# Kernel optimization log

Hardware: AMD Instinct MI355X
Metric: run time of the kernel (lower is better)

Reference implementation:

```python
import jax, jax.numpy as jnp
import numpy as np

N = 8192      # atoms
E = 4096      # edges (become transformer tokens)
E2 = 65536    # edges of second graph y
VOCAB = 119
DE = 200      # node_features == embedding_dim
D = 256
H = 8
L = 2
DFF = 2048


def _bn(x, g, b, eps=1e-6):
    m = x.mean(0)
    v = x.var(0)
    return (x - m) * jax.lax.rsqrt(v + eps) * g + b


def _ln(x, g, b, eps=1e-5):
    m = x.mean(-1, keepdims=True)
    v = ((x - m) ** 2).mean(-1, keepdims=True)
    return (x - m) * jax.lax.rsqrt(v + eps) * g + b


def _gcn(x, ei, W, b):
    # PyG GCNConv: add self loops, symmetric deg^-1/2 normalization
    n = x.shape[0]
    loop = jnp.arange(n)
    src = jnp.concatenate([ei[0], loop])
    dst = jnp.concatenate([ei[1], loop])
    deg = jax.ops.segment_sum(jnp.ones(src.shape[0], x.dtype), dst, num_segments=n)
    dinv = jnp.where(deg > 0, jax.lax.rsqrt(jnp.maximum(deg, 1e-12)), 0.0)
    msg = (x @ W)[src] * (dinv[src] * dinv[dst])[:, None]
    return jax.ops.segment_sum(msg, dst, num_segments=n) + b


def _mha(x, wi, bi, wo, bo):
    S, d = x.shape
    dh = d // H
    q, k, v = jnp.split(x @ wi + bi, 3, axis=1)
    q = q.reshape(S, H, dh)
    k = k.reshape(S, H, dh)
    v = v.reshape(S, H, dh)
    sc = jnp.einsum('qhd,khd->hqk', q, k) * (1.0 / np.sqrt(dh))
    a = jax.nn.softmax(sc, axis=-1)
    o = jnp.einsum('hqk,khd->qhd', a, v).reshape(S, d)
    return o @ wo + bo


def setup_inputs() -> dict:
    key = jax.random.key(0)
    ks = iter(jax.random.split(key, 64))
    nrm = lambda shape, s=0.05: jax.random.normal(next(ks), shape, jnp.float32) * s
    d = {}
    d['x'] = jax.random.randint(next(ks), (N,), 0, VOCAB)
    d['edge_index'] = jax.random.randint(next(ks), (2, E), 1, N + 1)  # 1-based, code subtracts 1
    d['pos'] = jax.random.normal(next(ks), (N, 3), jnp.float32)
    d['y'] = jax.random.randint(next(ks), (2, E2), 0, E)
    d['emb'] = nrm((VOCAB, DE), 1.0)
    d['fc1_w'] = nrm((1, DE))
    d['fc1_b'] = jnp.zeros((DE,), jnp.float32)
    d['bn4_g'] = jnp.ones((DE,), jnp.float32)
    d['bn4_b'] = jnp.zeros((DE,), jnp.float32)
    d['conv1_w'] = nrm((DE, D))
    d['conv1_b'] = jnp.zeros((D,), jnp.float32)
    d['conv2_w'] = nrm((D, D))
    d['conv2_b'] = jnp.zeros((D,), jnp.float32)
    for i in (1, 2, 3):
        d['bn%d_g' % i] = jnp.ones((D,), jnp.float32)
        d['bn%d_b' % i] = jnp.zeros((D,), jnp.float32)
    d['in_proj_w'] = nrm((L, D, 3 * D))
    d['in_proj_b'] = jnp.zeros((L, 3 * D), jnp.float32)
    d['out_proj_w'] = nrm((L, D, D))
    d['out_proj_b'] = jnp.zeros((L, D), jnp.float32)
    d['ln1_g'] = jnp.ones((L, D), jnp.float32)
    d['ln1_b'] = jnp.zeros((L, D), jnp.float32)
    d['ln2_g'] = jnp.ones((L, D), jnp.float32)
    d['ln2_b'] = jnp.zeros((L, D), jnp.float32)
    d['ff1_w'] = nrm((L, D, DFF))
    d['ff1_b'] = jnp.zeros((L, DFF), jnp.float32)
    d['ff2_w'] = nrm((L, DFF, D))
    d['ff2_b'] = jnp.zeros((L, D), jnp.float32)
    d['fc3_w'] = nrm((D, 1))
    d['fc3_b'] = jnp.zeros((1,), jnp.float32)
    d['fc4_w'] = nrm((D, 9))
    d['fc4_b'] = jnp.zeros((9,), jnp.float32)
    return d


def reference(x, edge_index, pos, y, emb, fc1_w, fc1_b, bn4_g, bn4_b,
              conv1_w, conv1_b, conv2_w, conv2_b,
              bn1_g, bn1_b, bn2_g, bn2_b, bn3_g, bn3_b,
              in_proj_w, in_proj_b, out_proj_w, out_proj_b,
              ln1_g, ln1_b, ln2_g, ln2_b, ff1_w, ff1_b, ff2_w, ff2_b,
              fc3_w, fc3_b, fc4_w, fc4_b):
    h = emb[x]                                   # [N, DE]
    ei = edge_index - 1
    row, col = ei[0], ei[1]
    ef = jnp.linalg.norm(pos[col] - pos[row], axis=1, keepdims=True)  # [E,1]
    ef = _bn(ef @ fc1_w + fc1_b, bn4_g, bn4_b)   # [E, DE]
    h = h[row] + h[col] + ef                     # [E, DE] edges -> tokens
    h = jax.nn.leaky_relu(_gcn(h, y, conv1_w, conv1_b))
    h = _bn(h, bn1_g, bn1_b)
    h = jax.nn.leaky_relu(h + _gcn(h, y, conv2_w, conv2_b))
    h = _bn(h, bn2_g, bn2_b)
    # post-norm TransformerEncoder (unbatched seq of length E), dropout=0
    for i in range(L):
        h = _ln(h + _mha(h, in_proj_w[i], in_proj_b[i], out_proj_w[i], out_proj_b[i]),
                ln1_g[i], ln1_b[i])
        ff = jax.nn.relu(h @ ff1_w[i] + ff1_b[i]) @ ff2_w[i] + ff2_b[i]
        h = _ln(h + ff, ln2_g[i], ln2_b[i])
    h = jax.nn.leaky_relu(h)
    h = _bn(h, bn3_g, bn3_b)
    sym_out = h @ fc3_w + fc3_b
    asym_out = h @ fc4_w + fc4_b
    return (sym_out, asym_out)
```

## Files before the change

### kernel.cpp

```cpp
#include <hip/hip_runtime.h>
#include <math.h>

#define ETOK 4096
#define NE2  65536
#define DEF  200
#define DM   256
#define NH   8
#define DH   32
#define DFFN 2048
#define NKS  4

#define QSCALE_LOG2E 0.25503474f

typedef __attribute__((ext_vector_type(8))) short bfrag8;
typedef __attribute__((ext_vector_type(4))) float f32x4;
typedef __attribute__((ext_vector_type(4))) short short4v;
typedef __attribute__((ext_vector_type(4))) unsigned int u32x4;

__device__ __forceinline__ unsigned short f2bf(float f) {
  union { float f; unsigned u; } v; v.f = f;
  unsigned u = v.u + 0x7fffu + ((v.u >> 16) & 1u);
  return (unsigned short)(u >> 16);
}
__device__ __forceinline__ float bf2f(unsigned short u) {
  union { unsigned u; float f; } v;
  v.u = ((unsigned)u) << 16;
  return v.f;
}
__device__ __forceinline__ unsigned cvt_pk_bf16(float lo, float hi) {
  unsigned r;
  asm("v_cvt_pk_bf16_f32 %0, %1, %2" : "=v"(r) : "v"(lo), "v"(hi));
  return r;
}

__device__ __forceinline__ float wave_sum(float v) {
#pragma unroll
  for (int off = 32; off > 0; off >>= 1) v += __shfl_xor(v, off);
  return v;
}
__device__ __forceinline__ float block_sum(float v, float* red) {
  v = wave_sum(v);
  int lane = threadIdx.x & 63, w = threadIdx.x >> 6;
  if (lane == 0) red[w] = v;
  __syncthreads();
  float t = red[0] + red[1] + red[2] + red[3];
  __syncthreads();
  return t;
}

__global__ void edge_deg_kernel(const int* __restrict__ ei, const float* __restrict__ pos,
                                float* __restrict__ ef0, float* __restrict__ stats,
                                const int* __restrict__ y, int* __restrict__ deg) {
  __shared__ float red[4];
  int e2 = blockIdx.x * 256 + threadIdx.x;
  atomicAdd(&deg[y[NE2 + e2]], 1);
  if (blockIdx.x < 16) {
    int e = blockIdx.x * 256 + threadIdx.x;
    int r = ei[e] - 1;
    int c = ei[ETOK + e] - 1;
    float dx = pos[c * 3 + 0] - pos[r * 3 + 0];
    float dy = pos[c * 3 + 1] - pos[r * 3 + 1];
    float dz = pos[c * 3 + 2] - pos[r * 3 + 2];
    float d = sqrtf(dx * dx + dy * dy + dz * dz);
    ef0[e] = d;
    float s = block_sum(d, red);
    float s2 = block_sum(d * d, red);
    if (threadIdx.x == 0) {
      atomicAdd(stats + 0, s);
      atomicAdd(stats + 1, s2);
    }
  }
}

__global__ void token_build_kernel(const int* __restrict__ x, const int* __restrict__ ei,
                                   const float* __restrict__ emb, const float* __restrict__ fc1_w,
                                   const float* __restrict__ bn4_g, const float* __restrict__ bn4_b,
                                   const float* __restrict__ ef0, const float* __restrict__ stats,
                                   unsigned short* __restrict__ tokbf) {
  int e = blockIdx.x;
  int j = threadIdx.x;
  float m = stats[0] * (1.0f / 4096.0f);
  float v = stats[1] * (1.0f / 4096.0f) - m * m;
  int xr = x[ei[e] - 1];
  int xc = x[ei[ETOK + e] - 1];
  float dd = ef0[e] - m;
  float val = 0.f;
  if (j < DEF) {
    float w = fc1_w[j];
    float s = w * rsqrtf(v * w * w + 1e-6f) * bn4_g[j];
    val = emb[(size_t)xr * DEF + j] + emb[(size_t)xc * DEF + j] + dd * s + bn4_b[j];
  }
  tokbf[(size_t)e * 256 + j] = f2bf(val);
}

__global__ void scan_kernel(const int* __restrict__ deg, int* __restrict__ off,
                            int* __restrict__ cursor, float* __restrict__ dinv) {
  __shared__ int part[256];
  int t = threadIdx.x;
  int v[16];
  int s = 0;
#pragma unroll
  for (int i = 0; i < 16; ++i) {
    v[i] = deg[t * 16 + i];
    s += v[i];
  }
  part[t] = s;
  __syncthreads();
  if (t == 0) {
    int a = 0;
#pragma unroll 1
    for (int i = 0; i < 256; ++i) {
      int tmp = part[i];
      part[i] = a;
      a += tmp;
    }
    off[4096] = a;
  }
  __syncthreads();
  int a = part[t];
#pragma unroll
  for (int i = 0; i < 16; ++i) {
    off[t * 16 + i] = a;
    cursor[t * 16 + i] = a;
    dinv[t * 16 + i] = rsqrtf((float)(v[i] + 1));
    a += v[i];
  }
}
__global__ void fill_kernel(const int* __restrict__ y, int* __restrict__ cursor,
                            int* __restrict__ srcl) {
  int e = blockIdx.x * 256 + threadIdx.x;
  int s = y[e];
  int d = y[NE2 + e];
  int slot = atomicAdd(&cursor[d], 1);
  srcl[slot] = s;
}

template <int RES, int ACT>
__global__ __launch_bounds__(256) void gather_kernel(const float* __restrict__ xw,
                                                     const int* __restrict__ off,
                                                     const int* __restrict__ srcl,
                                                     const float* __restrict__ dinv,
                                                     const float* __restrict__ bias,
                                                     const float* __restrict__ resid,
                                                     float* __restrict__ out) {
  __shared__ int slds[256];
  __shared__ float dlds[256];
  const int d = blockIdx.x;
  const int c = threadIdx.x;
  const int b0 = off[d], b1 = off[d + 1];
  const float dd = dinv[d];
  float acc = 0.f;
  for (int base = b0; base < b1; base += 256) {
    int n = min(256, b1 - base);
    __syncthreads();
    if (c < n) {
      int s = srcl[base + c];
      slds[c] = s;
      dlds[c] = dinv[s];
    }
    __syncthreads();
    for (int j = 0; j < n; ++j) {
      int s = slds[j];
      acc = fmaf(xw[(size_t)s * DM + c], dlds[j], acc);
    }
  }
  size_t idx = (size_t)d * DM + c;
  float v = bias[c] + xw[idx] * dd * dd + acc * dd;
  if (RES) v += resid[idx];
  if (ACT) v = v > 0.f ? v : 0.01f * v;
  out[idx] = v;
}

struct WEntry {
  const float* src;
  unsigned short* dst;
  int K, N, KP, tilesN, ntiles;
};
struct WPack {
  WEntry e[10];
};
__global__ __launch_bounds__(256) void wtrans_all_kernel(WPack p) {
  __shared__ float tl[32][33];
  int t = blockIdx.x;
  int i = 0;
  while (t >= p.e[i].ntiles) {
    t -= p.e[i].ntiles;
    ++i;
  }
  const WEntry w = p.e[i];
  int nb = (t % w.tilesN) * 32;
  int kb = (t / w.tilesN) * 32;
  int tx = threadIdx.x & 31, ty = threadIdx.x >> 5;
#pragma unroll
  for (int r = ty; r < 32; r += 8) {
    int k = kb + r, n = nb + tx;
    tl[r][tx] = (k < w.K && n < w.N) ? w.src[(size_t)k * w.N + n] : 0.f;
  }
  __syncthreads();
#pragma unroll
  for (int r = ty; r < 32; r += 8) {
    int n = nb + r, k = kb + tx;
    if (n < w.N) w.dst[(size_t)n * w.KP + k] = f2bf(tl[tx][r]);
  }
}

template <int BM, int BN, int OUTBF, int ACT, int QS, int VSPLIT>
__global__ __launch_bounds__(256) void mfma_gemm(const unsigned short* __restrict__ A,
                                                 const unsigned short* __restrict__ Bt,
                                                 const float* __restrict__ bias,
                                                 void* __restrict__ Cout, void* __restrict__ Cout2,
                                                 int M, int N, int K) {
  constexpr int BK = 64;
  constexpr int TM = BM / 32, TN = BN / 32;
  constexpr int ACH = BM / 32, BCH = BN / 32;
  __shared__ unsigned short Alds[BM * BK];
  __shared__ unsigned short Blds[BN * BK];
  const int tid = threadIdx.x;
  const int lane = tid & 63, wid = tid >> 6;
  const int g = lane >> 4, q = lane & 15;
  const int wr = wid >> 1, wc = wid & 1;
  const int m0 = blockIdx.y * BM, n0 = blockIdx.x * BN;

  f32x4 acc[TM][TN];
#pragma unroll
  for (int i = 0; i < TM; ++i)
#pragma unroll
    for (int j = 0; j < TN; ++j) acc[i][j] = (f32x4){0.f, 0.f, 0.f, 0.f};

  for (int k0 = 0; k0 < K; k0 += BK) {
    __syncthreads();
#pragma unroll
    for (int c = 0; c < ACH; ++c) {
      int chunk = wid * ACH + c;
      int row = chunk * 8 + (lane >> 3);
      int cb = ((lane & 7) * 16) ^ ((row & 7) << 4);
      const char* gp = (const char*)A + ((size_t)(m0 + row) * K + k0) * 2 + cb;
      __builtin_amdgcn_global_load_lds(
          (const __attribute__((address_space(1))) unsigned int*)gp,
          (__attribute__((address_space(3))) unsigned int*)(Alds + chunk * 512), 16, 0, 0);
    }
#pragma unroll
    for (int c = 0; c < BCH; ++c) {
      int chunk = wid * BCH + c;
      int row = chunk * 8 + (lane >> 3);
      int cb = ((lane & 7) * 16) ^ ((row & 7) << 4);
      const char* gp = (const char*)Bt + ((size_t)(n0 + row) * K + k0) * 2 + cb;
      __builtin_amdgcn_global_load_lds(
          (const __attribute__((address_space(1))) unsigned int*)gp,
          (__attribute__((address_space(3))) unsigned int*)(Blds + chunk * 512), 16, 0, 0);
    }
    __syncthreads();
#pragma unroll
    for (int ks = 0; ks < 2; ++ks) {
      bfrag8 af[TM], bfr[TN];
#pragma unroll
      for (int mi = 0; mi < TM; ++mi) {
        int row = wr * (BM / 2) + mi * 16 + q;
        int cb = (ks * 64 + g * 16) ^ ((row & 7) << 4);
        af[mi] = *(const bfrag8*)((const char*)Alds + row * 128 + cb);
      }
#pragma unroll
      for (int ni = 0; ni < TN; ++ni) {
        int row = wc * (BN / 2) + ni * 16 + q;
        int cb = (ks * 64 + g * 16) ^ ((row & 7) << 4);
        bfr[ni] = *(const bfrag8*)((const char*)Blds + row * 128 + cb);
      }
#pragma unroll
      for (int mi = 0; mi < TM; ++mi)
#pragma unroll
        for (int ni = 0; ni < TN; ++ni)
          acc[mi][ni] = __builtin_amdgcn_mfma_f32_16x16x32_bf16(af[mi], bfr[ni], acc[mi][ni], 0, 0, 0);
    }
  }
#pragma unroll
  for (int mi = 0; mi < TM; ++mi) {
    int row = m0 + wr * (BM / 2) + mi * 16 + g * 4;
#pragma unroll
    for (int ni = 0; ni < TN; ++ni) {
      int col = n0 + wc * (BN / 2) + ni * 16 + q;
      float bv = bias ? bias[col] : 0.f;
      if (VSPLIT && col >= 512) {
        short4v pkv;
#pragma unroll
        for (int r = 0; r < 4; ++r) pkv[r] = (short)f2bf(acc[mi][ni][r] + bv);
        *(short4v*)((unsigned short*)Cout2 + (size_t)(col - 512) * M + row) = pkv;
      } else {
#pragma unroll
        for (int r = 0; r < 4; ++r) {
          float v = acc[mi][ni][r] + bv;
          if (QS && col < DM) v *= QSCALE_LOG2E;
          if (ACT == 1) v = fmaxf(v, 0.f);
          if (OUTBF)
            ((unsigned short*)Cout)[(size_t)(row + r) * (VSPLIT ? 512 : N) + col] = f2bf(v);
          else
            ((float*)Cout)[(size_t)(row + r) * N + col] = v;
        }
      }
    }
  }
}

template <int LEAKY>
__global__ __launch_bounds__(256) void col_accum_kernel(const float* __restrict__ x,
                                                        float* __restrict__ colm,
                                                        float* __restrict__ colv) {
  int c = threadIdx.x;
  int r0 = blockIdx.x * 16;
  float s = 0.f, s2 = 0.f;
#pragma unroll
  for (int i = 0; i < 16; ++i) {
    float v = x[(size_t)(r0 + i) * DM + c];
    if (LEAKY) v = v > 0.f ? v : 0.01f * v;
    s += v;
    s2 += v * v;
  }
  atomicAdd(&colm[c], s);
  atomicAdd(&colv[c], s2);
}
template <int LEAKY>
__global__ void bn_apply_kernel(const float* __restrict__ x, const float* __restrict__ colm,
                                const float* __restrict__ colv, const float* __restrict__ g,
                                const float* __restrict__ b, float* __restrict__ outf,
                                unsigned short* __restrict__ outb, int C) {
  size_t i = (size_t)blockIdx.x * 256 + threadIdx.x;
  int c = (int)(i % C);
  float mean = colm[c] * (1.0f / 4096.0f);
  float var = colv[c] * (1.0f / 4096.0f) - mean * mean;
  float v0 = x[i];
  if (LEAKY) v0 = v0 > 0.f ? v0 : 0.01f * v0;
  float v = (v0 - mean) * rsqrtf(var + 1e-6f) * g[c] + b[c];
  outf[i] = v;
  if (outb) outb[i] = f2bf(v);
}

__global__ __launch_bounds__(256, 4) void attn_mfma_kernel(const unsigned short* __restrict__ qk,
                                                           const unsigned short* __restrict__ vt,
                                                           unsigned short* __restrict__ Opart,
                                                           float* __restrict__ Lpart) {
  const int h = blockIdx.y;
  const int qblk = blockIdx.x * 128;
  const int chunk = blockIdx.z;
  const int tid = threadIdx.x;
  const int wid = tid >> 6, lane = tid & 63;
  const int g = lane >> 4, q = lane & 15;

  __shared__ unsigned short Klds[2][64][40];
  __shared__ unsigned int Vtw[2][32][36];
  __shared__ unsigned short Plds[4][32][72];

  bfrag8 qfrag0, qfrag1;
  {
    const unsigned short* qp = qk + (size_t)(qblk + wid * 32 + q) * 512 + h * DH + g * 8;
    qfrag0 = *(const bfrag8*)qp;
    qfrag1 = *(const bfrag8*)(qp + 16 * 512);
  }
  const f32x4 zero = {0.f, 0.f, 0.f, 0.f};

  const int skey = tid >> 2;
  const int sdb = (tid & 3) * 8;
  const int sd = tid >> 3;
  const int sk4 = (tid & 7) * 4;

  const int kbeg = chunk * (ETOK / NKS);
  const int NT = (ETOK / NKS) / 64;

  const unsigned short* kptr = qk + (size_t)(kbeg + skey) * 512 + DM + h * DH + sdb;
  const unsigned short* vptr = vt + (size_t)(h * DH + sd) * ETOK + kbeg + sk4 * 2;

  bfrag8 kreg = *(const bfrag8*)kptr;
  kptr += (size_t)64 * 512;
  u32x4 vreg = *(const u32x4*)vptr;
  vptr += 64;

  float lsum0 = 0.f, lsum1 = 0.f;
  f32x4 o00 = zero, o01 = zero, o10 = zero, o11 = zero;

  for (int t = 0; t < NT; ++t) {
    const int buf = t & 1;
    *(bfrag8*)&Klds[buf][skey][sdb] = kreg;
    *(u32x4*)&Vtw[buf][sd][sk4] = vreg;
    __syncthreads();
    if (t + 1 < NT) {
      kreg = *(const bfrag8*)kptr;
      kptr += (size_t)64 * 512;
      vreg = *(const u32x4*)vptr;
      vptr += 64;
    }

    f32x4 st0[4], st1[4];
    __builtin_amdgcn_s_setprio(1);
#pragma unroll
    for (int tt = 0; tt < 4; ++tt) {
      bfrag8 kf = *(const bfrag8*)&Klds[buf][tt * 16 + q][g * 8];
      st0[tt] = __builtin_amdgcn_mfma_f32_16x16x32_bf16(kf, qfrag0, zero, 0, 0, 0);
      st1[tt] = __builtin_amdgcn_mfma_f32_16x16x32_bf16(kf, qfrag1, zero, 0, 0, 0);
    }
    __builtin_amdgcn_s_setprio(0);

    {
      float ps = 0.f;
#pragma unroll
      for (int tt = 0; tt < 4; ++tt) {
        float p0 = __builtin_exp2f(st0[tt][0]);
        float p1 = __builtin_exp2f(st0[tt][1]);
        float p2 = __builtin_exp2f(st0[tt][2]);
        float p3 = __builtin_exp2f(st0[tt][3]);
        ps += (p0 + p1) + (p2 + p3);
        uint2 w2;
        w2.x = cvt_pk_bf16(p0, p1);
        w2.y = cvt_pk_bf16(p2, p3);
        *(uint2*)&Plds[wid][q][tt * 16 + g * 4] = w2;
      }
      lsum0 += ps;
    }
    {
      float ps = 0.f;
#pragma unroll
      for (int tt = 0; tt < 4; ++tt) {
        float p0 = __builtin_exp2f(st1[tt][0]);
        float p1 = __builtin_exp2f(st1[tt][1]);
        float p2 = __builtin_exp2f(st1[tt][2]);
        float p3 = __builtin_exp2f(st1[tt][3]);
        ps += (p0 + p1) + (p2 + p3);
        uint2 w2;
        w2.x = cvt_pk_bf16(p0, p1);
        w2.y = cvt_pk_bf16(p2, p3);
        *(uint2*)&Plds[wid][16 + q][tt * 16 + g * 4] = w2;
      }
      lsum1 += ps;
    }

    __builtin_amdgcn_s_setprio(1);
#pragma unroll
    for (int kg = 0; kg < 2; ++kg) {
      bfrag8 vb0 = *(const bfrag8*)&Vtw[buf][q][kg * 16 + g * 4];
      bfrag8 vb1 = *(const bfrag8*)&Vtw[buf][16 + q][kg * 16 + g * 4];
      bfrag8 pa0 = *(const bfrag8*)&Plds[wid][q][kg * 32 + g * 8];
      bfrag8 pa1 = *(const bfrag8*)&Plds[wid][16 + q][kg * 32 + g * 8];
      o00 = __builtin_amdgcn_mfma_f32_16x16x32_bf16(pa0, vb0, o00, 0, 0, 0);
      o01 = __builtin_amdgcn_mfma_f32_16x16x32_bf16(pa0, vb1, o01, 0, 0, 0);
      o10 = __builtin_amdgcn_mfma_f32_16x16x32_bf16(pa1, vb0, o10, 0, 0, 0);
      o11 = __builtin_amdgcn_mfma_f32_16x16x32_bf16(pa1, vb1, o11, 0, 0, 0);
    }
    __builtin_amdgcn_s_setprio(0);
  }

  lsum0 += __shfl_xor(lsum0, 16);
  lsum0 += __shfl_xor(lsum0, 32);
  lsum1 += __shfl_xor(lsum1, 16);
  lsum1 += __shfl_xor(lsum1, 32);
#pragma unroll
  for (int r = 0; r < 4; ++r) {
    int row0 = qblk + wid * 32 + g * 4 + r;
    unsigned short* op0 = Opart + ((size_t)chunk * ETOK + row0) * DM + h * DH;
    op0[q] = f2bf(o00[r]);
    op0[16 + q] = f2bf(o01[r]);
    unsigned short* op1 = op0 + (size_t)16 * DM;
    op1[q] = f2bf(o10[r]);
    op1[16 + q] = f2bf(o11[r]);
  }
  if (lane < 16) {
    int row = qblk + wid * 32 + lane;
    Lpart[((size_t)chunk * ETOK + row) * NH + h] = lsum0;
    Lpart[((size_t)chunk * ETOK + row + 16) * NH + h] = lsum1;
  }
}

__global__ __launch_bounds__(256) void attn_combine_kernel(const unsigned short* __restrict__ Opart,
                                                           const float* __restrict__ Lpart,
                                                           unsigned short* __restrict__ out) {
  __shared__ float ls[NKS][NH];
  const int row = blockIdx.x;
  const int c = threadIdx.x;
  if (c < NKS * NH) {
    ls[c >> 3][c & 7] = Lpart[((size_t)(c >> 3) * ETOK + row) * NH + (c & 7)];
  }
  __syncthreads();
  const int h = c >> 5;
  float lstar = (ls[0][h] + ls[1][h]) + (ls[2][h] + ls[3][h]);
  float acc = 0.f;
#pragma unroll
  for (int ch = 0; ch < NKS; ++ch)
    acc += bf2f(Opart[((size_t)ch * ETOK + row) * DM + c]);
  out[(size_t)row * DM + c] = f2bf(acc / lstar);
}

__global__ void add_ln_kernel(const float* __restrict__ x, const float* __restrict__ r,
                              float* __restrict__ outf, unsigned short* __restrict__ outb,
                              const float* __restrict__ g, const float* __restrict__ b) {
  __shared__ float red[4];
  int row = blockIdx.x, t = threadIdx.x;
  size_t idx = (size_t)row * DM + t;
  float v = x[idx] + r[idx];
  float mean = block_sum(v, red) * (1.0f / 256.0f);
  float dv = v - mean;
  float var = block_sum(dv * dv, red) * (1.0f / 256.0f);
  float o = dv * rsqrtf(var + 1e-5f) * g[t] + b[t];
  outf[idx] = o;
  outb[idx] = f2bf(o);
}

__global__ void head_kernel(const float* __restrict__ h, const float* __restrict__ colm,
                            const float* __restrict__ colv, const float* __restrict__ bng,
                            const float* __restrict__ bnb, const float* __restrict__ fc3w,
                            const float* __restrict__ fc3b, const float* __restrict__ fc4w,
                            const float* __restrict__ fc4b, float* __restrict__ out) {
  int wave = threadIdx.x >> 6, lane = threadIdx.x & 63;
  int tok = blockIdx.x * 4 + wave;
  const float* hr = h + (size_t)tok * DM;
  float hv[4];
#pragma unroll
  for (int i = 0; i < 4; ++i) {
    int col = lane * 4 + i;
    float v = hr[col];
    v = v > 0.f ? v : 0.01f * v;
    float mean = colm[col] * (1.0f / 4096.0f);
    float var = colv[col] * (1.0f / 4096.0f) - mean * mean;
    hv[i] = (v - mean) * rsqrtf(var + 1e-6f) * bng[col] + bnb[col];
  }
  float acc = 0.f;
#pragma unroll
  for (int i = 0; i < 4; ++i) acc += hv[i] * fc3w[lane * 4 + i];
  acc = wave_sum(acc);
  if (lane == 0) out[tok] = acc + fc3b[0];
#pragma unroll
  for (int j = 0; j < 9; ++j) {
    float a = 0.f;
#pragma unroll
    for (int i = 0; i < 4; ++i) a += hv[i] * fc4w[(lane * 4 + i) * 9 + j];
    a = wave_sum(a);
    if (lane == 0) out[ETOK + (size_t)tok * 9 + j] = a + fc4b[j];
  }
}

extern "C" void kernel_launch(void* const* d_in, const int* in_sizes, int n_in,
                              void* d_out, int out_size, void* d_ws, size_t ws_size,
                              hipStream_t stream) {
  const int* x = (const int*)d_in[0];
  const int* edge_index = (const int*)d_in[1];
  const float* pos = (const float*)d_in[2];
  const int* y = (const int*)d_in[3];
  const float* emb = (const float*)d_in[4];
  const float* fc1_w = (const float*)d_in[5];
  const float* bn4_g = (const float*)d_in[7];
  const float* bn4_b = (const float*)d_in[8];
  const float* conv1_w = (const float*)d_in[9];
  const float* conv1_b = (const float*)d_in[10];
  const float* conv2_w = (const float*)d_in[11];
  const float* conv2_b = (const float*)d_in[12];
  const float* bn1_g = (const float*)d_in[13];
  const float* bn1_b = (const float*)d_in[14];
  const float* bn2_g = (const float*)d_in[15];
  const float* bn2_b = (const float*)d_in[16];
  const float* bn3_g = (const float*)d_in[17];
  const float* bn3_b = (const float*)d_in[18];
  const float* ipw = (const float*)d_in[19];
  const float* ipb = (const float*)d_in[20];
  const float* opw = (const float*)d_in[21];
  const float* opb = (const float*)d_in[22];
  const float* ln1_g = (const float*)d_in[23];
  const float* ln1_b = (const float*)d_in[24];
  const float* ln2_g = (const float*)d_in[25];
  const float* ln2_b = (const float*)d_in[26];
  const float* ff1w = (const float*)d_in[27];
  const float* ff1b = (const float*)d_in[28];
  const float* ff2w = (const float*)d_in[29];
  const float* ff2b = (const float*)d_in[30];
  const float* fc3w = (const float*)d_in[31];
  const float* fc3b = (const float*)d_in[32];
  const float* fc4w = (const float*)d_in[33];
  const float* fc4b = (const float*)d_in[34];
  float* outp = (float*)d_out;

  char* wsp = (char*)d_ws;
  auto alloc = [&](size_t bytes) {
    void* p = (void*)wsp;
    wsp += (bytes + 255) & ~(size_t)255;
    return p;
  };
  unsigned short* big_bf = (unsigned short*)alloc((size_t)ETOK * DFFN * 2);
  unsigned short* qk_bf = (unsigned short*)alloc((size_t)ETOK * 512 * 2);
  unsigned short* vt_bf = (unsigned short*)alloc((size_t)DM * ETOK * 2);
  unsigned short* attno = (unsigned short*)alloc((size_t)ETOK * DM * 2);
  unsigned short* h_bf = (unsigned short*)alloc((size_t)ETOK * DM * 2);
  unsigned short* tok_bf = (unsigned short*)alloc((size_t)ETOK * 256 * 2);
  float* hf = (float*)alloc((size_t)ETOK * DM * 4);
  float* t1 = (float*)alloc((size_t)ETOK * DM * 4);
  float* t2 = (float*)alloc((size_t)ETOK * DM * 4);
  unsigned short* Opart = (unsigned short*)alloc((size_t)NKS * ETOK * DM * 2);
  float* Lpart = (float*)alloc((size_t)NKS * ETOK * NH * 4);
  unsigned short* c1wt = (unsigned short*)alloc(256 * 256 * 2);
  unsigned short* c2wt = (unsigned short*)alloc(256 * 256 * 2);
  unsigned short* ipwt = (unsigned short*)alloc((size_t)2 * 768 * 256 * 2);
  unsigned short* opwt = (unsigned short*)alloc((size_t)2 * 256 * 256 * 2);
  unsigned short* f1wt = (unsigned short*)alloc((size_t)2 * 2048 * 256 * 2);
  unsigned short* f2wt = (unsigned short*)alloc((size_t)2 * 256 * 2048 * 2);
  float* ef0 = (float*)alloc(ETOK * 4);
  float* dinv = (float*)alloc(ETOK * 4);
  int* off = (int*)alloc((ETOK + 1) * 4);
  int* cursor = (int*)alloc(ETOK * 4);
  int* srcl = (int*)alloc(NE2 * 4);
  char* z0 = wsp;
  float* stats = (float*)alloc(8 * 4);
  float* colm = (float*)alloc(3 * DM * 4);
  float* colv = (float*)alloc(3 * DM * 4);
  int* deg = (int*)alloc(ETOK * 4);
  size_t zlen = (char*)wsp - z0;

  hipMemsetAsync(z0, 0, zlen, stream);

  WPack wp;
  int ntot = 0;
  auto went = [&](int i, const float* src, unsigned short* dst, int K, int N, int KP) {
    wp.e[i].src = src;
    wp.e[i].dst = dst;
    wp.e[i].K = K;
    wp.e[i].N = N;
    wp.e[i].KP = KP;
    wp.e[i].tilesN = (N + 31) / 32;
    wp.e[i].ntiles = ((N + 31) / 32) * (KP / 32);
    ntot += wp.e[i].ntiles;
  };
  went(0, conv1_w, c1wt, 200, 256, 256);
  went(1, conv2_w, c2wt, 256, 256, 256);
  went(2, ipw, ipwt, 256, 768, 256);
  went(3, ipw + (size_t)256 * 768, ipwt + (size_t)768 * 256, 256, 768, 256);
  went(4, opw, opwt, 256, 256, 256);
  went(5, opw + (size_t)256 * 256, opwt + (size_t)256 * 256, 256, 256, 256);
  went(6, ff1w, f1wt, 256, 2048, 256);
  went(7, ff1w + (size_t)256 * 2048, f1wt + (size_t)2048 * 256, 256, 2048, 256);
  went(8, ff2w, f2wt, 2048, 256, 2048);
  went(9, ff2w + (size_t)2048 * 256, f2wt + (size_t)256 * 2048, 2048, 256, 2048);
  wtrans_all_kernel<<<ntot, 256, 0, stream>>>(wp);

  edge_deg_kernel<<<NE2 / 256, 256, 0, stream>>>(edge_index, pos, ef0, stats, y, deg);
  scan_kernel<<<1, 256, 0, stream>>>(deg, off, cursor, dinv);
  fill_kernel<<<NE2 / 256, 256, 0, stream>>>(y, cursor, srcl);
  token_build_kernel<<<ETOK, 256, 0, stream>>>(x, edge_index, emb, fc1_w, bn4_g, bn4_b, ef0,
                                               stats, tok_bf);

  mfma_gemm<32, 32, 0, 0, 0, 0><<<dim3(8, 128), 256, 0, stream>>>(tok_bf, c1wt, nullptr, t1,
                                                                  nullptr, ETOK, DM, 256);
  gather_kernel<0, 1><<<ETOK, 256, 0, stream>>>(t1, off, srcl, dinv, conv1_b, nullptr, t2);
  col_accum_kernel<0><<<ETOK / 16, 256, 0, stream>>>(t2, colm, colv);
  bn_apply_kernel<0><<<ETOK * DM / 256, 256, 0, stream>>>(t2, colm, colv, bn1_g, bn1_b, hf, h_bf, DM);

  mfma_gemm<32, 32, 0, 0, 0, 0><<<dim3(8, 128), 256, 0, stream>>>(h_bf, c2wt, nullptr, t1,
                                                                  nullptr, ETOK, DM, 256);
  gather_kernel<1, 1><<<ETOK, 256, 0, stream>>>(t1, off, srcl, dinv, conv2_b, hf, t2);
  col_accum_kernel<0><<<ETOK / 16, 256, 0, stream>>>(t2, colm + DM, colv + DM);
  bn_apply_kernel<0><<<ETOK * DM / 256, 256, 0, stream>>>(t2, colm + DM, colv + DM, bn2_g, bn2_b,
                                                          hf, h_bf, DM);

  for (int i = 0; i < 2; ++i) {
    mfma_gemm<32, 32, 1, 0, 1, 1><<<dim3(24, 128), 256, 0, stream>>>(
        h_bf, ipwt + (size_t)i * 768 * 256, ipb + (size_t)i * 768, qk_bf, vt_bf, ETOK, 768, 256);
    attn_mfma_kernel<<<dim3(ETOK / 128, NH, NKS), 256, 0, stream>>>(qk_bf, vt_bf, Opart, Lpart);
    attn_combine_kernel<<<ETOK, 256, 0, stream>>>(Opart, Lpart, attno);
    mfma_gemm<32, 32, 0, 0, 0, 0><<<dim3(8, 128), 256, 0, stream>>>(
        attno, opwt + (size_t)i * 256 * 256, opb + (size_t)i * DM, t2, nullptr, ETOK, DM, 256);
    add_ln_kernel<<<ETOK, 256, 0, stream>>>(t2, hf, hf, h_bf, ln1_g + (size_t)i * DM,
                                            ln1_b + (size_t)i * DM);
    mfma_gemm<64, 64, 1, 1, 0, 0><<<dim3(32, 64), 256, 0, stream>>>(
        h_bf, f1wt + (size_t)i * 2048 * 256, ff1b + (size_t)i * DFFN, big_bf, nullptr, ETOK, DFFN, 256);
    mfma_gemm<32, 32, 0, 0, 0, 0><<<dim3(8, 128), 256, 0, stream>>>(
        big_bf, f2wt + (size_t)i * 256 * 2048, ff2b + (size_t)i * DM, t2, nullptr, ETOK, DM, 2048);
    add_ln_kernel<<<ETOK, 256, 0, stream>>>(t2, hf, hf, h_bf, ln2_g + (size_t)i * DM,
                                            ln2_b + (size_t)i * DM);
  }

  col_accum_kernel<1><<<ETOK / 16, 256, 0, stream>>>(hf, colm + 2 * DM, colv + 2 * DM);
  head_kernel<<<ETOK / 4, 256, 0, stream>>>(hf, colm + 2 * DM, colv + 2 * DM, bn3_g, bn3_b,
                                            fc3w, fc3b, fc4w, fc4b, outp);
}
```

Before: 327.8 us.

## Shrink attention LDS and registers, compute row sums via MFMA, split keys eight ways

```diff
diff --git a/kernel.cpp b/kernel.cpp
--- a/kernel.cpp
+++ b/kernel.cpp
@@ -8,7 +8,7 @@
 #define NH   8
 #define DH   32
 #define DFFN 2048
-#define NKS  4
+#define NKS  8
 
 #define QSCALE_LOG2E 0.25503474f
 
@@ -333,7 +333,7 @@
   if (outb) outb[i] = f2bf(v);
 }
 
-__global__ __launch_bounds__(256, 4) void attn_mfma_kernel(const unsigned short* __restrict__ qk,
+__global__ __launch_bounds__(256, 6) void attn_mfma_kernel(const unsigned short* __restrict__ qk,
                                                            const unsigned short* __restrict__ vt,
                                                            unsigned short* __restrict__ Opart,
                                                            float* __restrict__ Lpart) {
@@ -344,9 +344,9 @@
   const int wid = tid >> 6, lane = tid & 63;
   const int g = lane >> 4, q = lane & 15;
 
-  __shared__ unsigned short Klds[2][64][40];
-  __shared__ unsigned int Vtw[2][32][36];
-  __shared__ unsigned short Plds[4][32][72];
+  __shared__ unsigned short Klds[64][40];
+  __shared__ unsigned int Vtw[32][36];
+  __shared__ unsigned short Plds[4][32][40];
 
   bfrag8 qfrag0, qfrag1;
   {
@@ -354,6 +354,9 @@
     qfrag0 = *(const bfrag8*)qp;
     qfrag1 = *(const bfrag8*)(qp + 16 * 512);
   }
+  bfrag8 ones;
+#pragma unroll
+  for (int i = 0; i < 8; ++i) ones[i] = (short)0x3F80;
   const f32x4 zero = {0.f, 0.f, 0.f, 0.f};
 
   const int skey = tid >> 2;
@@ -372,13 +375,12 @@
   u32x4 vreg = *(const u32x4*)vptr;
   vptr += 64;
 
-  float lsum0 = 0.f, lsum1 = 0.f;
   f32x4 o00 = zero, o01 = zero, o10 = zero, o11 = zero;
+  f32x4 ol0 = zero, ol1 = zero;
 
   for (int t = 0; t < NT; ++t) {
-    const int buf = t & 1;
-    *(bfrag8*)&Klds[buf][skey][sdb] = kreg;
-    *(u32x4*)&Vtw[buf][sd][sk4] = vreg;
+    *(bfrag8*)&Klds[skey][sdb] = kreg;
+    *(u32x4*)&Vtw[sd][sk4] = vreg;
     __syncthreads();
     if (t + 1 < NT) {
       kreg = *(const bfrag8*)kptr;
@@ -387,68 +389,54 @@
       vptr += 64;
     }
 
-    f32x4 st0[4], st1[4];
-    __builtin_amdgcn_s_setprio(1);
-#pragma unroll
-    for (int tt = 0; tt < 4; ++tt) {
-      bfrag8 kf = *(const bfrag8*)&Klds[buf][tt * 16 + q][g * 8];
-      st0[tt] = __builtin_amdgcn_mfma_f32_16x16x32_bf16(kf, qfrag0, zero, 0, 0, 0);
-      st1[tt] = __builtin_amdgcn_mfma_f32_16x16x32_bf16(kf, qfrag1, zero, 0, 0, 0);
-    }
-    __builtin_amdgcn_s_setprio(0);
-
-    {
-      float ps = 0.f;
-#pragma unroll
-      for (int tt = 0; tt < 4; ++tt) {
-        float p0 = __builtin_exp2f(st0[tt][0]);
-        float p1 = __builtin_exp2f(st0[tt][1]);
-        float p2 = __builtin_exp2f(st0[tt][2]);
-        float p3 = __builtin_exp2f(st0[tt][3]);
-        ps += (p0 + p1) + (p2 + p3);
+#pragma unroll
+    for (int kg = 0; kg < 2; ++kg) {
+      f32x4 s0a, s0b, s1a, s1b;
+      __builtin_amdgcn_s_setprio(1);
+      {
+        bfrag8 kfa = *(const bfrag8*)&Klds[(2 * kg) * 16 + q][g * 8];
+        bfrag8 kfb = *(const bfrag8*)&Klds[(2 * kg + 1) * 16 + q][g * 8];
+        s0a = __builtin_amdgcn_mfma_f32_16x16x32_bf16(kfa, qfrag0, zero, 0, 0, 0);
+        s1a = __builtin_amdgcn_mfma_f32_16x16x32_bf16(kfa, qfrag1, zero, 0, 0, 0);
+        s0b = __builtin_amdgcn_mfma_f32_16x16x32_bf16(kfb, qfrag0, zero, 0, 0, 0);
+        s1b = __builtin_amdgcn_mfma_f32_16x16x32_bf16(kfb, qfrag1, zero, 0, 0, 0);
+      }
+      __builtin_amdgcn_s_setprio(0);
+
+      {
         uint2 w2;
-        w2.x = cvt_pk_bf16(p0, p1);
-        w2.y = cvt_pk_bf16(p2, p3);
-        *(uint2*)&Plds[wid][q][tt * 16 + g * 4] = w2;
+        w2.x = cvt_pk_bf16(__builtin_exp2f(s0a[0]), __builtin_exp2f(s0a[1]));
+        w2.y = cvt_pk_bf16(__builtin_exp2f(s0a[2]), __builtin_exp2f(s0a[3]));
+        *(uint2*)&Plds[wid][q][g * 4] = w2;
+        w2.x = cvt_pk_bf16(__builtin_exp2f(s0b[0]), __builtin_exp2f(s0b[1]));
+        w2.y = cvt_pk_bf16(__builtin_exp2f(s0b[2]), __builtin_exp2f(s0b[3]));
+        *(uint2*)&Plds[wid][q][16 + g * 4] = w2;
+        w2.x = cvt_pk_bf16(__builtin_exp2f(s1a[0]), __builtin_exp2f(s1a[1]));
+        w2.y = cvt_pk_bf16(__builtin_exp2f(s1a[2]), __builtin_exp2f(s1a[3]));
+        *(uint2*)&Plds[wid][16 + q][g * 4] = w2;
+        w2.x = cvt_pk_bf16(__builtin_exp2f(s1b[0]), __builtin_exp2f(s1b[1]));
+        w2.y = cvt_pk_bf16(__builtin_exp2f(s1b[2]), __builtin_exp2f(s1b[3]));
+        *(uint2*)&Plds[wid][16 + q][16 + g * 4] = w2;
       }
-      lsum0 += ps;
-    }
-    {
-      float ps = 0.f;
-#pragma unroll
-      for (int tt = 0; tt < 4; ++tt) {
-        float p0 = __builtin_exp2f(st1[tt][0]);
-        float p1 = __builtin_exp2f(st1[tt][1]);
-        float p2 = __builtin_exp2f(st1[tt][2]);
-        float p3 = __builtin_exp2f(st1[tt][3]);
-        ps += (p0 + p1) + (p2 + p3);
-        uint2 w2;
-        w2.x = cvt_pk_bf16(p0, p1);
-        w2.y = cvt_pk_bf16(p2, p3);
-        *(uint2*)&Plds[wid][16 + q][tt * 16 + g * 4] = w2;
+
+      __builtin_amdgcn_s_setprio(1);
+      {
+        bfrag8 pa0 = *(const bfrag8*)&Plds[wid][q][g * 8];
+        bfrag8 pa1 = *(const bfrag8*)&Plds[wid][16 + q][g * 8];
+        bfrag8 vb0 = *(const bfrag8*)&Vtw[q][kg * 16 + g * 4];
+        bfrag8 vb1 = *(const bfrag8*)&Vtw[16 + q][kg * 16 + g * 4];
+        o00 = __builtin_amdgcn_mfma_f32_16x16x32_bf16(pa0, vb0, o00, 0, 0, 0);
+        o01 = __builtin_amdgcn_mfma_f32_16x16x32_bf16(pa0, vb1, o01, 0, 0, 0);
+        o10 = __builtin_amdgcn_mfma_f32_16x16x32_bf16(pa1, vb0, o10, 0, 0, 0);
+        o11 = __builtin_amdgcn_mfma_f32_16x16x32_bf16(pa1, vb1, o11, 0, 0, 0);
+        ol0 = __builtin_amdgcn_mfma_f32_16x16x32_bf16(pa0, ones, ol0, 0, 0, 0);
+        ol1 = __builtin_amdgcn_mfma_f32_16x16x32_bf16(pa1, ones, ol1, 0, 0, 0);
       }
-      lsum1 += ps;
-    }
-
-    __builtin_amdgcn_s_setprio(1);
-#pragma unroll
-    for (int kg = 0; kg < 2; ++kg) {
-      bfrag8 vb0 = *(const bfrag8*)&Vtw[buf][q][kg * 16 + g * 4];
-      bfrag8 vb1 = *(const bfrag8*)&Vtw[buf][16 + q][kg * 16 + g * 4];
-      bfrag8 pa0 = *(const bfrag8*)&Plds[wid][q][kg * 32 + g * 8];
-      bfrag8 pa1 = *(const bfrag8*)&Plds[wid][16 + q][kg * 32 + g * 8];
-      o00 = __builtin_amdgcn_mfma_f32_16x16x32_bf16(pa0, vb0, o00, 0, 0, 0);
-      o01 = __builtin_amdgcn_mfma_f32_16x16x32_bf16(pa0, vb1, o01, 0, 0, 0);
-      o10 = __builtin_amdgcn_mfma_f32_16x16x32_bf16(pa1, vb0, o10, 0, 0, 0);
-      o11 = __builtin_amdgcn_mfma_f32_16x16x32_bf16(pa1, vb1, o11, 0, 0, 0);
-    }
-    __builtin_amdgcn_s_setprio(0);
-  }
-
-  lsum0 += __shfl_xor(lsum0, 16);
-  lsum0 += __shfl_xor(lsum0, 32);
-  lsum1 += __shfl_xor(lsum1, 16);
-  lsum1 += __shfl_xor(lsum1, 32);
+      __builtin_amdgcn_s_setprio(0);
+    }
+    __syncthreads();
+  }
+
 #pragma unroll
   for (int r = 0; r < 4; ++r) {
     int row0 = qblk + wid * 32 + g * 4 + r;
@@ -459,10 +447,13 @@
     op1[q] = f2bf(o10[r]);
     op1[16 + q] = f2bf(o11[r]);
   }
-  if (lane < 16) {
-    int row = qblk + wid * 32 + lane;
-    Lpart[((size_t)chunk * ETOK + row) * NH + h] = lsum0;
-    Lpart[((size_t)chunk * ETOK + row + 16) * NH + h] = lsum1;
+  if (q == 0) {
+#pragma unroll
+    for (int r = 0; r < 4; ++r) {
+      int row = qblk + wid * 32 + g * 4 + r;
+      Lpart[((size_t)chunk * ETOK + row) * NH + h] = ol0[r];
+      Lpart[((size_t)chunk * ETOK + row + 16) * NH + h] = ol1[r];
+    }
   }
 }
 
@@ -477,11 +468,12 @@
   }
   __syncthreads();
   const int h = c >> 5;
-  float lstar = (ls[0][h] + ls[1][h]) + (ls[2][h] + ls[3][h]);
-  float acc = 0.f;
-#pragma unroll
-  for (int ch = 0; ch < NKS; ++ch)
+  float lstar = 0.f, acc = 0.f;
+#pragma unroll
+  for (int ch = 0; ch < NKS; ++ch) {
+    lstar += ls[ch][h];
     acc += bf2f(Opart[((size_t)ch * ETOK + row) * DM + c]);
+  }
   out[(size_t)row * DM + c] = f2bf(acc / lstar);
 }
 
```

Measured after the change: 321.7 us, median of 2. No clear change (-1.9%).
